# Performance work log

Hardware: AMD Instinct MI355X
Metric: run time of the kernel (lower is better)

## Reference

```python
import jax, jax.numpy as jnp
import numpy as np

N_NODES = 100000
IN_CH = 256
EMBED = 256
N_EDGES = 300000
EPS = 1e-5


def _glorot(key, shape):
    fan_in, fan_out = shape[0], shape[1]
    lim = (6.0 / (fan_in + fan_out)) ** 0.5
    return jax.random.uniform(key, shape, jnp.float32, -lim, lim)


def setup_inputs() -> dict:
    key = jax.random.key(0)
    ks = jax.random.split(key, 16)
    inp = {}
    inp['node_feat'] = jax.random.normal(ks[0], (N_NODES, IN_CH), jnp.float32)
    inp['src'] = jax.random.randint(ks[1], (N_EDGES,), 0, N_NODES, jnp.int32)
    inp['dst'] = jax.random.randint(ks[2], (N_EDGES,), 0, N_NODES, jnp.int32)
    inp['neg'] = jax.random.randint(ks[3], (N_EDGES,), 0, N_NODES, jnp.int32)
    # GCNConv weights (x @ W + b), 3 layers
    inp['W1'] = _glorot(ks[4], (IN_CH, EMBED)); inp['b1'] = jnp.zeros((EMBED,), jnp.float32)
    inp['W2'] = _glorot(ks[5], (EMBED, EMBED)); inp['b2'] = jnp.zeros((EMBED,), jnp.float32)
    inp['W3'] = _glorot(ks[6], (EMBED, EMBED)); inp['b3'] = jnp.zeros((EMBED,), jnp.float32)
    # BatchNorm affine params (2 BN layers)
    inp['g1'] = jnp.ones((EMBED,), jnp.float32); inp['be1'] = jnp.zeros((EMBED,), jnp.float32)
    inp['g2'] = jnp.ones((EMBED,), jnp.float32); inp['be2'] = jnp.zeros((EMBED,), jnp.float32)
    # LinkPredictor MLP
    inp['fc1_w'] = _glorot(ks[7], (2 * EMBED, EMBED)); inp['fc1_b'] = jnp.zeros((EMBED,), jnp.float32)
    inp['fc2_w'] = _glorot(ks[8], (EMBED, 1)); inp['fc2_b'] = jnp.zeros((1,), jnp.float32)
    return inp


def gcn_conv(x, W, b, src, dst, n):
    # PyG GCNConv: out = D^{-1/2} (A + I) D^{-1/2} (x @ W) + b
    xw = x @ W
    loops = jnp.arange(n, dtype=src.dtype)
    src_l = jnp.concatenate([src, loops])
    dst_l = jnp.concatenate([dst, loops])
    deg = jax.ops.segment_sum(jnp.ones_like(dst_l, jnp.float32), dst_l, num_segments=n)
    dinv = jnp.where(deg > 0, jax.lax.rsqrt(deg), 0.0)
    norm = dinv[src_l] * dinv[dst_l]  # [E+N]
    msg = norm[:, None] * xw[src_l]   # [E+N, d]
    out = jax.ops.segment_sum(msg, dst_l, num_segments=n)
    return out + b


def batch_norm(x, g, b):
    # training-mode BN over node dim, biased variance (torch semantics)
    mu = jnp.mean(x, axis=0)
    var = jnp.mean((x - mu) ** 2, axis=0)
    return (x - mu) * jax.lax.rsqrt(var + EPS) * g + b


def link_pred(z_a, z_b, fc1_w, fc1_b, fc2_w, fc2_b):
    h = jnp.concatenate([z_a, z_b], axis=1) @ fc1_w + fc1_b
    h = jax.nn.relu(h)
    return jax.nn.sigmoid(h @ fc2_w + fc2_b).reshape(-1)


def reference(node_feat, src, dst, neg, W1, b1, W2, b2, W3, b3, g1, be1, g2, be2, fc1_w, fc1_b, fc2_w, fc2_b):
    n = node_feat.shape[0]
    # encoder (dropout p used only in training; inference/deterministic here)
    x = gcn_conv(node_feat, W1, b1, src, dst, n)
    x = jax.nn.relu(batch_norm(x, g1, be1))
    x = gcn_conv(x, W2, b2, src, dst, n)
    x = jax.nn.relu(batch_norm(x, g2, be2))
    z = gcn_conv(x, W3, b3, src, dst, n)
    z_src, z_dst, z_neg = z[src], z[dst], z[neg]
    pos_out = link_pred(z_src, z_dst, fc1_w, fc1_b, fc2_w, fc2_b)
    neg_out = link_pred(z_src, z_neg, fc1_w, fc1_b, fc2_w, fc2_b)
    return (pos_out, neg_out)
```

## Files before the change

kernel.cpp:

```cpp
#include <hip/hip_runtime.h>
#include <hip/hip_bf16.h>

#define N_NODES 100000
#define N_EDGES 300000
#define CH 256
#define EPS 1e-5f
#define AGG_BLOCKS 3125
#define Y_TILES 782
#define Y_TILES_PAD 784

typedef __hip_bfloat16 bf16;
typedef __attribute__((ext_vector_type(8))) short bf16x8_t;
typedef __attribute__((ext_vector_type(4))) float f32x4_t;

__device__ __forceinline__ unsigned short f2bf(float f) {
    bf16 h = __float2bfloat16(f);
    return __builtin_bit_cast(unsigned short, h);
}
__device__ __forceinline__ float bf2f(unsigned short u) {
    unsigned int x = ((unsigned int)u) << 16;
    return __builtin_bit_cast(float, x);
}
__device__ __forceinline__ float bflo(unsigned int w) {
    return __builtin_bit_cast(float, w << 16);
}
__device__ __forceinline__ float bfhi(unsigned int w) {
    return __builtin_bit_cast(float, w & 0xffff0000u);
}
__device__ __forceinline__ unsigned pack2(float a, float b) {
    return (unsigned)f2bf(a) | ((unsigned)f2bf(b) << 16);
}
__device__ __forceinline__ void store_val(bf16* p, float v) { *p = __float2bfloat16(v); }

__device__ __forceinline__ void async_copy16(const void* g, void* l) {
    __builtin_amdgcn_global_load_lds((const __attribute__((address_space(1))) void*)g,
                                     (__attribute__((address_space(3))) void*)l, 16, 0, 0);
}

__global__ void k_zero_int(int* __restrict__ p, int n) {
    int i = blockIdx.x * 256 + threadIdx.x;
    if (i < n) p[i] = 0;
}
__global__ void k_count_deg(const int* __restrict__ dst, int* __restrict__ deg) {
    int e = blockIdx.x * 256 + threadIdx.x;
    if (e < N_EDGES) atomicAdd(&deg[dst[e]], 1);
}
__global__ void k_dinv_from_deg(const int* __restrict__ deg, float* __restrict__ dinv) {
    int i = blockIdx.x * 256 + threadIdx.x;
    if (i < N_NODES) dinv[i] = rsqrtf((float)(deg[i] + 1));
}
__global__ void k_block_sums(const int* __restrict__ deg, int* __restrict__ bsum) {
    __shared__ int s[256];
    int t = threadIdx.x;
    int i = blockIdx.x * 256 + t;
    s[t] = (i < N_NODES) ? deg[i] : 0;
    __syncthreads();
    for (int off = 128; off > 0; off >>= 1) {
        if (t < off) s[t] += s[t + off];
        __syncthreads();
    }
    if (t == 0) bsum[blockIdx.x] = s[0];
}
__global__ void k_scan_bsums(int* __restrict__ bsum, int nb) {
    __shared__ int s[512];
    int t = threadIdx.x;
    int v = (t < nb) ? bsum[t] : 0;
    s[t] = v;
    __syncthreads();
    for (int off = 1; off < 512; off <<= 1) {
        int u = (t >= off) ? s[t - off] : 0;
        __syncthreads();
        s[t] += u;
        __syncthreads();
    }
    if (t < nb) bsum[t] = s[t] - v;
}
__global__ void k_row_ptr(const int* __restrict__ deg, const int* __restrict__ bsum,
                          int* __restrict__ row_ptr) {
    __shared__ int s[256];
    int t = threadIdx.x;
    int i = blockIdx.x * 256 + t;
    int v = (i < N_NODES) ? deg[i] : 0;
    s[t] = v;
    __syncthreads();
    for (int off = 1; off < 256; off <<= 1) {
        int u = (t >= off) ? s[t - off] : 0;
        __syncthreads();
        s[t] += u;
        __syncthreads();
    }
    if (i < N_NODES) row_ptr[i] = bsum[blockIdx.x] + s[t] - v;
    if (blockIdx.x == 0 && t == 0) row_ptr[N_NODES] = N_EDGES;
}
__global__ void k_scatter(const int* __restrict__ src, const int* __restrict__ dst,
                          const int* __restrict__ row_ptr, int* __restrict__ cursor,
                          const float* __restrict__ dinv,
                          int* __restrict__ col, float* __restrict__ wedge,
                          int* __restrict__ eid, int* __restrict__ rowid) {
    int e = blockIdx.x * 256 + threadIdx.x;
    if (e < N_EDGES) {
        int d = dst[e], s = src[e];
        int p = atomicAdd(&cursor[d], 1);
        int idx = row_ptr[d] + p;
        col[idx] = s;
        wedge[idx] = dinv[d] * dinv[s];
        eid[idx] = e;
        rowid[idx] = d;
    }
}

__global__ void k_transpose_all(const float* __restrict__ W1, const float* __restrict__ W2,
                                bf16* __restrict__ wt) {
    int which = blockIdx.x >> 8;
    int idx = ((blockIdx.x & 255) << 8) + threadIdx.x;
    int n = idx >> 8, k = idx & 255;
    const float* W = which ? W2 : W1;
    wt[(size_t)which * 65536 + (size_t)n * 256 + k] =
        __float2bfloat16(W[(size_t)k * 256 + n]);
}

__global__ void k_fuse_w(const float* __restrict__ W3, const float* __restrict__ fc1w,
                         bf16* __restrict__ wtf) {
    __shared__ float w3row[256];
    int k = blockIdx.x;
    int n = threadIdx.x;
    if (n < 256) w3row[n] = W3[(size_t)k * 256 + n];
    __syncthreads();
    int nc = n & 255;
    size_t ro = (n < 256) ? 0 : 256;
    float acc = 0.f;
#pragma unroll 4
    for (int j = 0; j < 256; ++j)
        acc += w3row[j] * fc1w[(ro + j) * 256 + nc];
    wtf[(size_t)n * 256 + k] = __float2bfloat16(acc);
}
__global__ void k_fuse_bias(const float* __restrict__ b3, const float* __restrict__ fc1w,
                            const float* __restrict__ fc1b, float* __restrict__ bout) {
    int n = threadIdx.x;
    int nc = n & 255;
    size_t ro = (n < 256) ? 0 : 256;
    float acc = (n < 256) ? fc1b[n] : 0.f;
#pragma unroll 4
    for (int j = 0; j < 256; ++j)
        acc += b3[j] * fc1w[(ro + j) * 256 + nc];
    bout[n] = acc;
}

__global__ void k_cast_bf16_v4(const float* __restrict__ x, unsigned short* __restrict__ y) {
    int i = blockIdx.x * 256 + threadIdx.x;
    float4 v = ((const float4*)x)[i];
    ushort4 o;
    o.x = f2bf(v.x); o.y = f2bf(v.y); o.z = f2bf(v.z); o.w = f2bf(v.w);
    ((ushort4*)y)[i] = o;
}

template <int NX, bool BIAS, bool STATS>
__global__ __launch_bounds__(256) void k_gemm_mfma(const bf16* __restrict__ A,
                                                   const bf16* __restrict__ Bt,
                                                   bf16* __restrict__ C, int M, int ldc,
                                                   const float* __restrict__ bias,
                                                   float* __restrict__ part) {
    constexpr int LOG2NX = (NX == 4) ? 2 : 1;
    int id = blockIdx.x;
    int rg = (id & 7) + 8 * (id >> (3 + LOG2NX));
    int ct = (id >> 3) & (NX - 1);
    if (rg >= Y_TILES) return;
    const int row0 = rg * 128;
    const int col0 = ct * 128;

    __shared__ bf16 As[128 * 64];
    __shared__ bf16 Bs[128 * 64];
    __shared__ float sS[2][128];
    __shared__ float sQ[2][128];
    const int tid = threadIdx.x;
    const int lane = tid & 63;
    const int w = tid >> 6;
    const int wr = w >> 1, wc = w & 1;
    const int lr = lane & 15, quad = lane >> 4;

    f32x4_t acc[4][4] = {};

    for (int k0 = 0; k0 < 256; k0 += 64) {
#pragma unroll
        for (int i = 0; i < 4; ++i) {
            int j = i * 256 + tid;
            int r = j >> 3, c = j & 7;
            int gk = ((c ^ (r & 7)) << 3);
            int gr = row0 + r; gr = gr < M ? gr : M - 1;
            async_copy16(A + (size_t)gr * 256 + k0 + gk, (void*)(As + j * 8));
            async_copy16(Bt + (size_t)(col0 + r) * 256 + k0 + gk, (void*)(Bs + j * 8));
        }
        __syncthreads();
#pragma unroll
        for (int ks = 0; ks < 2; ++ks) {
            bf16x8_t af[4], bfr[4];
#pragma unroll
            for (int mi = 0; mi < 4; ++mi) {
                int m = wr * 64 + mi * 16 + lr;
                int c = (ks * 4 + quad) ^ (m & 7);
                af[mi] = *(const bf16x8_t*)(As + m * 64 + c * 8);
            }
#pragma unroll
            for (int ni = 0; ni < 4; ++ni) {
                int n = wc * 64 + ni * 16 + lr;
                int c = (ks * 4 + quad) ^ (n & 7);
                bfr[ni] = *(const bf16x8_t*)(Bs + n * 64 + c * 8);
            }
#pragma unroll
            for (int mi = 0; mi < 4; ++mi)
#pragma unroll
                for (int ni = 0; ni < 4; ++ni)
                    acc[mi][ni] = __builtin_amdgcn_mfma_f32_16x16x32_bf16(
                        af[mi], bfr[ni], acc[mi][ni], 0, 0, 0);
        }
        __syncthreads();
    }
#pragma unroll
    for (int ni = 0; ni < 4; ++ni) {
        int colg = col0 + wc * 64 + ni * 16 + lr;
        float bv = BIAS ? bias[colg] : 0.f;
#pragma unroll
        for (int mi = 0; mi < 4; ++mi)
#pragma unroll
            for (int r = 0; r < 4; ++r) acc[mi][ni][r] += bv;
    }
    if (STATS) {
        float cs[4] = {}, cq[4] = {};
#pragma unroll
        for (int mi = 0; mi < 4; ++mi)
#pragma unroll
            for (int r = 0; r < 4; ++r) {
                int row = row0 + wr * 64 + mi * 16 + quad * 4 + r;
                if (row < M) {
#pragma unroll
                    for (int ni = 0; ni < 4; ++ni) {
                        float v = acc[mi][ni][r];
                        cs[ni] += v;
                        cq[ni] += v * v;
                    }
                }
            }
#pragma unroll
        for (int ni = 0; ni < 4; ++ni) {
            cs[ni] += __shfl_xor(cs[ni], 16, 64);
            cs[ni] += __shfl_xor(cs[ni], 32, 64);
            cq[ni] += __shfl_xor(cq[ni], 16, 64);
            cq[ni] += __shfl_xor(cq[ni], 32, 64);
        }
        if (quad == 0) {
#pragma unroll
            for (int ni = 0; ni < 4; ++ni) {
                int cc = wc * 64 + ni * 16 + lr;
                sS[wr][cc] = cs[ni];
                sQ[wr][cc] = cq[ni];
            }
        }
        __syncthreads();
        if (tid < 128) {
            float ss = sS[0][tid] + sS[1][tid];
            float qq = sQ[0][tid] + sQ[1][tid];
            int cg = col0 + tid;
            part[(size_t)rg * 512 + cg] = ss;
            part[(size_t)rg * 512 + 256 + cg] = qq;
        }
    }
#pragma unroll
    for (int mi = 0; mi < 4; ++mi) {
#pragma unroll
        for (int r = 0; r < 4; ++r) {
            int row = row0 + wr * 64 + mi * 16 + quad * 4 + r;
            if (row < M) {
#pragma unroll
                for (int ni = 0; ni < 4; ++ni) {
                    int colg = col0 + wc * 64 + ni * 16 + lr;
                    store_val(C + (size_t)row * ldc + colg, acc[mi][ni][r]);
                }
            }
        }
    }
}

template <bool BN>
__device__ __forceinline__ void expand8(uint4 m, const float* sc, const float* sh, float* r) {
    r[0] = bflo(m.x); r[1] = bfhi(m.x); r[2] = bflo(m.y); r[3] = bfhi(m.y);
    r[4] = bflo(m.z); r[5] = bfhi(m.z); r[6] = bflo(m.w); r[7] = bfhi(m.w);
    if (BN) {
#pragma unroll
        for (int i = 0; i < 8; ++i) r[i] = fmaxf(r[i] * sc[i] + sh[i], 0.f);
    }
}

template <bool BN>
__global__ __launch_bounds__(256) void k_agg_csr(const unsigned short* __restrict__ x,
                                                 const int* __restrict__ row_ptr,
                                                 const int* __restrict__ col,
                                                 const float* __restrict__ wedge,
                                                 const float* __restrict__ dinv,
                                                 const float* __restrict__ scale,
                                                 const float* __restrict__ shift,
                                                 bf16* __restrict__ out) {
    int g = threadIdx.x >> 5, lh = threadIdx.x & 31;
    int base = blockIdx.x * 32 + g * 4;
    const uint4* xv = (const uint4*)x;
    float sc[8], sh[8];
    if (BN) {
        float4 a = ((const float4*)scale)[lh * 2];
        float4 b = ((const float4*)scale)[lh * 2 + 1];
        float4 c = ((const float4*)shift)[lh * 2];
        float4 d = ((const float4*)shift)[lh * 2 + 1];
        sc[0] = a.x; sc[1] = a.y; sc[2] = a.z; sc[3] = a.w;
        sc[4] = b.x; sc[5] = b.y; sc[6] = b.z; sc[7] = b.w;
        sh[0] = c.x; sh[1] = c.y; sh[2] = c.z; sh[3] = c.w;
        sh[4] = d.x; sh[5] = d.y; sh[6] = d.z; sh[7] = d.w;
    }
#pragma unroll
    for (int n = 0; n < 4; ++n) {
        int node = base + n;
        int beg = row_ptr[node], end = row_ptr[node + 1];
        float dv = dinv[node];
        float s2 = dv * dv;
        uint4 xr = xv[(size_t)node * 32 + lh];
        float rs[8];
        expand8<BN>(xr, sc, sh, rs);
        float a[8];
#pragma unroll
        for (int t = 0; t < 8; ++t) a[t] = s2 * rs[t];
        int i = beg;
        for (; i + 2 <= end; i += 2) {
            int sa = col[i], sb = col[i + 1];
            float wa = wedge[i], wb = wedge[i + 1];
            uint4 ma = xv[(size_t)sa * 32 + lh];
            uint4 mb = xv[(size_t)sb * 32 + lh];
            float ra[8], rb[8];
            expand8<BN>(ma, sc, sh, ra);
            expand8<BN>(mb, sc, sh, rb);
#pragma unroll
            for (int t = 0; t < 8; ++t) a[t] += wa * ra[t] + wb * rb[t];
        }
        if (i < end) {
            int sa = col[i];
            float wa = wedge[i];
            uint4 ma = xv[(size_t)sa * 32 + lh];
            float ra[8];
            expand8<BN>(ma, sc, sh, ra);
#pragma unroll
            for (int t = 0; t < 8; ++t) a[t] += wa * ra[t];
        }
        uint4 o;
        o.x = pack2(a[0], a[1]); o.y = pack2(a[2], a[3]);
        o.z = pack2(a[4], a[5]); o.w = pack2(a[6], a[7]);
        ((uint4*)(out + (size_t)node * CH))[lh] = o;
    }
}

__global__ __launch_bounds__(256) void k_bn_finalize(const float* __restrict__ part,
                                                     const float* __restrict__ g,
                                                     const float* __restrict__ be,
                                                     float* __restrict__ scale,
                                                     float* __restrict__ shift) {
    int wave = threadIdx.x >> 6, lane = threadIdx.x & 63;
    int c = blockIdx.x * 4 + wave;
    float s = 0.f, q = 0.f;
    for (int j = lane; j < Y_TILES; j += 64) {
        s += part[(size_t)j * 512 + c];
        q += part[(size_t)j * 512 + 256 + c];
    }
#pragma unroll
    for (int off = 32; off > 0; off >>= 1) {
        s += __shfl_down(s, off, 64);
        q += __shfl_down(q, off, 64);
    }
    if (lane == 0) {
        float mu = s * (1.0f / N_NODES);
        float var = q * (1.0f / N_NODES) - mu * mu;
        float sc = g[c] * rsqrtf(var + EPS);
        scale[c] = sc;
        shift[c] = be[c] - mu * sc;
    }
}

__global__ __launch_bounds__(256) void k_edge_score(
        const unsigned short* __restrict__ uv,
        const int* __restrict__ col, const int* __restrict__ eid,
        const int* __restrict__ rowid, const int* __restrict__ neg,
        const float* __restrict__ fc2_w, const float* __restrict__ fc2_b,
        float* __restrict__ out) {
    constexpr int NWG = 18750;
    constexpr int Q = NWG / 8, R = NWG % 8;
    int bid = blockIdx.x;
    int xcd = bid & 7, ord = bid >> 3;
    int swz = ((xcd < R) ? xcd * (Q + 1) : R * (Q + 1) + (xcd - R) * Q) + ord;
    int wave = threadIdx.x >> 6, lane = threadIdx.x & 63;
    int qtr = lane >> 4, l = lane & 15;
    int i = swz * 16 + wave * 4 + qtr;
    int s = col[i], d = rowid[i], e = eid[i];
    int g = neg[e];
    const uint4* uvv = (const uint4*)uv;
    uint4 u0 = uvv[(size_t)s * 64 + l * 2];
    uint4 u1 = uvv[(size_t)s * 64 + l * 2 + 1];
    uint4 p0 = uvv[(size_t)d * 64 + 32 + l * 2];
    uint4 p1 = uvv[(size_t)d * 64 + 33 + l * 2];
    uint4 n0 = uvv[(size_t)g * 64 + 32 + l * 2];
    uint4 n1 = uvv[(size_t)g * 64 + 33 + l * 2];
    float4 w0 = ((const float4*)fc2_w)[l * 4];
    float4 w1 = ((const float4*)fc2_w)[l * 4 + 1];
    float4 w2 = ((const float4*)fc2_w)[l * 4 + 2];
    float4 w3 = ((const float4*)fc2_w)[l * 4 + 3];

    float t0 = bflo(u0.x), t1 = bfhi(u0.x), t2 = bflo(u0.y), t3 = bfhi(u0.y);
    float t4 = bflo(u0.z), t5 = bfhi(u0.z), t6 = bflo(u0.w), t7 = bfhi(u0.w);
    float t8 = bflo(u1.x), t9 = bfhi(u1.x), ta = bflo(u1.y), tb = bfhi(u1.y);
    float tc = bflo(u1.z), td = bfhi(u1.z), te = bflo(u1.w), tf = bfhi(u1.w);

    float accp =
        fmaxf(t0 + bflo(p0.x), 0.f) * w0.x + fmaxf(t1 + bfhi(p0.x), 0.f) * w0.y +
        fmaxf(t2 + bflo(p0.y), 0.f) * w0.z + fmaxf(t3 + bfhi(p0.y), 0.f) * w0.w +
        fmaxf(t4 + bflo(p0.z), 0.f) * w1.x + fmaxf(t5 + bfhi(p0.z), 0.f) * w1.y +
        fmaxf(t6 + bflo(p0.w), 0.f) * w1.z + fmaxf(t7 + bfhi(p0.w), 0.f) * w1.w +
        fmaxf(t8 + bflo(p1.x), 0.f) * w2.x + fmaxf(t9 + bfhi(p1.x), 0.f) * w2.y +
        fmaxf(ta + bflo(p1.y), 0.f) * w2.z + fmaxf(tb + bfhi(p1.y), 0.f) * w2.w +
        fmaxf(tc + bflo(p1.z), 0.f) * w3.x + fmaxf(td + bfhi(p1.z), 0.f) * w3.y +
        fmaxf(te + bflo(p1.w), 0.f) * w3.z + fmaxf(tf + bfhi(p1.w), 0.f) * w3.w;
    float accn =
        fmaxf(t0 + bflo(n0.x), 0.f) * w0.x + fmaxf(t1 + bfhi(n0.x), 0.f) * w0.y +
        fmaxf(t2 + bflo(n0.y), 0.f) * w0.z + fmaxf(t3 + bfhi(n0.y), 0.f) * w0.w +
        fmaxf(t4 + bflo(n0.z), 0.f) * w1.x + fmaxf(t5 + bfhi(n0.z), 0.f) * w1.y +
        fmaxf(t6 + bflo(n0.w), 0.f) * w1.z + fmaxf(t7 + bfhi(n0.w), 0.f) * w1.w +
        fmaxf(t8 + bflo(n1.x), 0.f) * w2.x + fmaxf(t9 + bfhi(n1.x), 0.f) * w2.y +
        fmaxf(ta + bflo(n1.y), 0.f) * w2.z + fmaxf(tb + bfhi(n1.y), 0.f) * w2.w +
        fmaxf(tc + bflo(n1.z), 0.f) * w3.x + fmaxf(td + bfhi(n1.z), 0.f) * w3.y +
        fmaxf(te + bflo(n1.w), 0.f) * w3.z + fmaxf(tf + bfhi(n1.w), 0.f) * w3.w;
#pragma unroll
    for (int off = 8; off > 0; off >>= 1) {
        accp += __shfl_down(accp, off, 64);
        accn += __shfl_down(accn, off, 64);
    }
    if (l == 0) {
        float bb = fc2_b[0];
        out[e] = 1.0f / (1.0f + expf(-(accp + bb)));
        out[N_EDGES + e] = 1.0f / (1.0f + expf(-(accn + bb)));
    }
}

extern "C" void kernel_launch(void* const* d_in, const int* in_sizes, int n_in,
                              void* d_out, int out_size, void* d_ws, size_t ws_size,
                              hipStream_t stream) {
    const float* node_feat = (const float*)d_in[0];
    const int* src = (const int*)d_in[1];
    const int* dst = (const int*)d_in[2];
    const int* neg = (const int*)d_in[3];
    const float* W1 = (const float*)d_in[4];  const float* b1 = (const float*)d_in[5];
    const float* W2 = (const float*)d_in[6];  const float* b2 = (const float*)d_in[7];
    const float* W3 = (const float*)d_in[8];  const float* b3 = (const float*)d_in[9];
    const float* g1 = (const float*)d_in[10]; const float* be1 = (const float*)d_in[11];
    const float* g2 = (const float*)d_in[12]; const float* be2 = (const float*)d_in[13];
    const float* fc1_w = (const float*)d_in[14]; const float* fc1_b = (const float*)d_in[15];
    const float* fc2_w = (const float*)d_in[16]; const float* fc2_b = (const float*)d_in[17];
    float* out = (float*)d_out;

    const size_t NF = (size_t)N_NODES * CH;
    bf16* UV = (bf16*)d_ws;
    bf16* Xbf = UV + 2 * NF;
    bf16* XwBf = Xbf + NF;
    bf16* wt = XwBf + NF;
    float* dinv = (float*)(wt + 4 * 65536);
    float* bnpart = dinv + N_NODES;
    float* scale = bnpart + (size_t)Y_TILES * 512;
    float* shift = scale + CH;
    float* b3fc = shift + CH;
    float* wedge = b3fc + 512;
    int* ideg = (int*)(wedge + N_EDGES);
    int* cursor = ideg + N_NODES;
    int* row_ptr = cursor + N_NODES;
    int* col = row_ptr + N_NODES + 1;
    int* eid = col + N_EDGES;
    int* rowid = eid + N_EDGES;
    int* bsum = rowid + N_EDGES;
    (void)ws_size;

    int gemmBlocks = 2 * Y_TILES_PAD;
    int uvBlocks = 4 * Y_TILES_PAD;
    int nodeBlocks = (N_NODES + 255) / 256;
    int edgeBlocks = (N_EDGES + 255) / 256;
    int v4Blocks = (int)(NF / 4 / 256);
    int scoreBlocks = N_EDGES / 16;

    k_zero_int<<<(2 * N_NODES + 255) / 256, 256, 0, stream>>>(ideg, 2 * N_NODES);
    k_count_deg<<<edgeBlocks, 256, 0, stream>>>(dst, ideg);
    k_dinv_from_deg<<<nodeBlocks, 256, 0, stream>>>(ideg, dinv);
    k_block_sums<<<nodeBlocks, 256, 0, stream>>>(ideg, bsum);
    k_scan_bsums<<<1, 512, 0, stream>>>(bsum, nodeBlocks);
    k_row_ptr<<<nodeBlocks, 256, 0, stream>>>(ideg, bsum, row_ptr);
    k_scatter<<<edgeBlocks, 256, 0, stream>>>(src, dst, row_ptr, cursor, dinv, col, wedge,
                                              eid, rowid);

    k_transpose_all<<<512, 256, 0, stream>>>(W1, W2, wt);
    k_fuse_w<<<256, 512, 0, stream>>>(W3, fc1_w, wt + 2 * 65536);
    k_fuse_bias<<<1, 512, 0, stream>>>(b3, fc1_w, fc1_b, b3fc);

    k_cast_bf16_v4<<<v4Blocks, 256, 0, stream>>>(node_feat, (unsigned short*)Xbf);

    k_agg_csr<false><<<AGG_BLOCKS, 256, 0, stream>>>((unsigned short*)Xbf, row_ptr, col,
                                                     wedge, dinv, nullptr, nullptr, XwBf);
    k_gemm_mfma<2, true, true><<<gemmBlocks, 256, 0, stream>>>(XwBf, wt, Xbf, N_NODES, 256,
                                                               b1, bnpart);
    k_bn_finalize<<<64, 256, 0, stream>>>(bnpart, g1, be1, scale, shift);

    k_agg_csr<true><<<AGG_BLOCKS, 256, 0, stream>>>((unsigned short*)Xbf, row_ptr, col,
                                                    wedge, dinv, scale, shift, XwBf);
    k_gemm_mfma<2, true, true><<<gemmBlocks, 256, 0, stream>>>(XwBf, wt + 65536, Xbf,
                                                               N_NODES, 256, b2, bnpart);
    k_bn_finalize<<<64, 256, 0, stream>>>(bnpart, g2, be2, scale, shift);

    k_agg_csr<true><<<AGG_BLOCKS, 256, 0, stream>>>((unsigned short*)Xbf, row_ptr, col,
                                                    wedge, dinv, scale, shift, XwBf);
    k_gemm_mfma<4, true, false><<<uvBlocks, 256, 0, stream>>>(XwBf, wt + 2 * 65536, UV,
                                                              N_NODES, 512, b3fc, nullptr);

    k_edge_score<<<scoreBlocks, 256, 0, stream>>>((unsigned short*)UV, col, eid, rowid, neg,
                                                  fc2_w, fc2_b, out);
}
```

Baseline: 566.0 us.

## Fuse input cast into first GEMM and move layer-1 BN stats into aggregation

The first layer now runs GEMM before aggregation, and the GEMM converts the fp32 node features to bf16 while loading them. That removes the separate cast kernel and its round trip through memory. Bias and the batch-norm partial sums move into the aggregation kernel, which adds shared-memory reductions and partials per aggregation block, so finalize reads more partials. Small setup kernels (dinv, fused bias) are folded into other launches to cut launch count; the synchronous fp32 A loads in the GEMM lose the async copy path.

Result: no change. 558.8 us (-1.3%).

```diff
diff --git a/kernel.cpp b/kernel.cpp
--- a/kernel.cpp
+++ b/kernel.cpp
@@ -17,10 +17,6 @@
     bf16 h = __float2bfloat16(f);
     return __builtin_bit_cast(unsigned short, h);
 }
-__device__ __forceinline__ float bf2f(unsigned short u) {
-    unsigned int x = ((unsigned int)u) << 16;
-    return __builtin_bit_cast(float, x);
-}
 __device__ __forceinline__ float bflo(unsigned int w) {
     return __builtin_bit_cast(float, w << 16);
 }
@@ -45,15 +41,14 @@
     int e = blockIdx.x * 256 + threadIdx.x;
     if (e < N_EDGES) atomicAdd(&deg[dst[e]], 1);
 }
-__global__ void k_dinv_from_deg(const int* __restrict__ deg, float* __restrict__ dinv) {
-    int i = blockIdx.x * 256 + threadIdx.x;
-    if (i < N_NODES) dinv[i] = rsqrtf((float)(deg[i] + 1));
-}
-__global__ void k_block_sums(const int* __restrict__ deg, int* __restrict__ bsum) {
+__global__ void k_block_sums(const int* __restrict__ deg, int* __restrict__ bsum,
+                             float* __restrict__ dinv) {
     __shared__ int s[256];
     int t = threadIdx.x;
     int i = blockIdx.x * 256 + t;
-    s[t] = (i < N_NODES) ? deg[i] : 0;
+    int v = (i < N_NODES) ? deg[i] : 0;
+    s[t] = v;
+    if (i < N_NODES) dinv[i] = rsqrtf((float)(v + 1));
     __syncthreads();
     for (int off = 128; off > 0; off >>= 1) {
         if (t < off) s[t] += s[t + off];
@@ -120,42 +115,33 @@
 }
 
 __global__ void k_fuse_w(const float* __restrict__ W3, const float* __restrict__ fc1w,
-                         bf16* __restrict__ wtf) {
+                         const float* __restrict__ b3, const float* __restrict__ fc1b,
+                         bf16* __restrict__ wtf, float* __restrict__ bout) {
+    int n = threadIdx.x;
+    int nc = n & 255;
+    size_t ro = (n < 256) ? 0 : 256;
+    if (blockIdx.x == 256) {
+        float acc = (n < 256) ? fc1b[n] : 0.f;
+#pragma unroll 4
+        for (int j = 0; j < 256; ++j)
+            acc += b3[j] * fc1w[(ro + j) * 256 + nc];
+        bout[n] = acc;
+        return;
+    }
     __shared__ float w3row[256];
     int k = blockIdx.x;
-    int n = threadIdx.x;
     if (n < 256) w3row[n] = W3[(size_t)k * 256 + n];
     __syncthreads();
-    int nc = n & 255;
-    size_t ro = (n < 256) ? 0 : 256;
     float acc = 0.f;
 #pragma unroll 4
     for (int j = 0; j < 256; ++j)
         acc += w3row[j] * fc1w[(ro + j) * 256 + nc];
     wtf[(size_t)n * 256 + k] = __float2bfloat16(acc);
 }
-__global__ void k_fuse_bias(const float* __restrict__ b3, const float* __restrict__ fc1w,
-                            const float* __restrict__ fc1b, float* __restrict__ bout) {
-    int n = threadIdx.x;
-    int nc = n & 255;
-    size_t ro = (n < 256) ? 0 : 256;
-    float acc = (n < 256) ? fc1b[n] : 0.f;
-#pragma unroll 4
-    for (int j = 0; j < 256; ++j)
-        acc += b3[j] * fc1w[(ro + j) * 256 + nc];
-    bout[n] = acc;
-}
-
-__global__ void k_cast_bf16_v4(const float* __restrict__ x, unsigned short* __restrict__ y) {
-    int i = blockIdx.x * 256 + threadIdx.x;
-    float4 v = ((const float4*)x)[i];
-    ushort4 o;
-    o.x = f2bf(v.x); o.y = f2bf(v.y); o.z = f2bf(v.z); o.w = f2bf(v.w);
-    ((ushort4*)y)[i] = o;
-}
-
-template <int NX, bool BIAS, bool STATS>
+
+template <int NX, bool BIAS, bool STATS, bool F32A>
 __global__ __launch_bounds__(256) void k_gemm_mfma(const bf16* __restrict__ A,
+                                                   const float* __restrict__ Af,
                                                    const bf16* __restrict__ Bt,
                                                    bf16* __restrict__ C, int M, int ldc,
                                                    const float* __restrict__ bias,
@@ -187,7 +173,16 @@
             int r = j >> 3, c = j & 7;
             int gk = ((c ^ (r & 7)) << 3);
             int gr = row0 + r; gr = gr < M ? gr : M - 1;
-            async_copy16(A + (size_t)gr * 256 + k0 + gk, (void*)(As + j * 8));
+            if (F32A) {
+                const float4* ap = (const float4*)(Af + (size_t)gr * 256 + k0 + gk);
+                float4 fa = ap[0], fb = ap[1];
+                uint4 o;
+                o.x = pack2(fa.x, fa.y); o.y = pack2(fa.z, fa.w);
+                o.z = pack2(fb.x, fb.y); o.w = pack2(fb.z, fb.w);
+                *(uint4*)(As + (size_t)j * 8) = o;
+            } else {
+                async_copy16(A + (size_t)gr * 256 + k0 + gk, (void*)(As + j * 8));
+            }
             async_copy16(Bt + (size_t)(col0 + r) * 256 + k0 + gk, (void*)(Bs + j * 8));
         }
         __syncthreads();
@@ -290,7 +285,7 @@
     }
 }
 
-template <bool BN>
+template <bool BN, bool STATS>
 __global__ __launch_bounds__(256) void k_agg_csr(const unsigned short* __restrict__ x,
                                                  const int* __restrict__ row_ptr,
                                                  const int* __restrict__ col,
@@ -298,11 +293,15 @@
                                                  const float* __restrict__ dinv,
                                                  const float* __restrict__ scale,
                                                  const float* __restrict__ shift,
-                                                 bf16* __restrict__ out) {
+                                                 const float* __restrict__ bias,
+                                                 bf16* __restrict__ out,
+                                                 float* __restrict__ part) {
+    __shared__ float sred[8][256];
+    __shared__ float qred[8][256];
     int g = threadIdx.x >> 5, lh = threadIdx.x & 31;
     int base = blockIdx.x * 32 + g * 4;
     const uint4* xv = (const uint4*)x;
-    float sc[8], sh[8];
+    float sc[8], sh[8], bs[8];
     if (BN) {
         float4 a = ((const float4*)scale)[lh * 2];
         float4 b = ((const float4*)scale)[lh * 2 + 1];
@@ -313,6 +312,13 @@
         sh[0] = c.x; sh[1] = c.y; sh[2] = c.z; sh[3] = c.w;
         sh[4] = d.x; sh[5] = d.y; sh[6] = d.z; sh[7] = d.w;
     }
+    if (STATS) {
+        float4 e = ((const float4*)bias)[lh * 2];
+        float4 f = ((const float4*)bias)[lh * 2 + 1];
+        bs[0] = e.x; bs[1] = e.y; bs[2] = e.z; bs[3] = e.w;
+        bs[4] = f.x; bs[5] = f.y; bs[6] = f.z; bs[7] = f.w;
+    }
+    float s8[8] = {}, q8[8] = {};
 #pragma unroll
     for (int n = 0; n < 4; ++n) {
         int node = base + n;
@@ -346,22 +352,47 @@
 #pragma unroll
             for (int t = 0; t < 8; ++t) a[t] += wa * ra[t];
         }
+        if (STATS) {
+#pragma unroll
+            for (int t = 0; t < 8; ++t) {
+                a[t] += bs[t];
+                s8[t] += a[t];
+                q8[t] += a[t] * a[t];
+            }
+        }
         uint4 o;
         o.x = pack2(a[0], a[1]); o.y = pack2(a[2], a[3]);
         o.z = pack2(a[4], a[5]); o.w = pack2(a[6], a[7]);
         ((uint4*)(out + (size_t)node * CH))[lh] = o;
     }
+    if (STATS) {
+#pragma unroll
+        for (int j = 0; j < 8; ++j) {
+            sred[g][lh * 8 + j] = s8[j];
+            qred[g][lh * 8 + j] = q8[j];
+        }
+        __syncthreads();
+        int t = threadIdx.x;
+        float ss = 0.f, qq = 0.f;
+#pragma unroll
+        for (int gg = 0; gg < 8; ++gg) {
+            ss += sred[gg][t];
+            qq += qred[gg][t];
+        }
+        part[(size_t)blockIdx.x * 512 + t] = ss;
+        part[(size_t)blockIdx.x * 512 + 256 + t] = qq;
+    }
 }
 
 __global__ __launch_bounds__(256) void k_bn_finalize(const float* __restrict__ part,
                                                      const float* __restrict__ g,
                                                      const float* __restrict__ be,
                                                      float* __restrict__ scale,
-                                                     float* __restrict__ shift) {
+                                                     float* __restrict__ shift, int npart) {
     int wave = threadIdx.x >> 6, lane = threadIdx.x & 63;
     int c = blockIdx.x * 4 + wave;
     float s = 0.f, q = 0.f;
-    for (int j = lane; j < Y_TILES; j += 64) {
+    for (int j = lane; j < npart; j += 64) {
         s += part[(size_t)j * 512 + c];
         q += part[(size_t)j * 512 + 256 + c];
     }
@@ -465,7 +496,7 @@
     bf16* wt = XwBf + NF;
     float* dinv = (float*)(wt + 4 * 65536);
     float* bnpart = dinv + N_NODES;
-    float* scale = bnpart + (size_t)Y_TILES * 512;
+    float* scale = bnpart + (size_t)AGG_BLOCKS * 512;
     float* shift = scale + CH;
     float* b3fc = shift + CH;
     float* wedge = b3fc + 512;
@@ -482,40 +513,35 @@
     int uvBlocks = 4 * Y_TILES_PAD;
     int nodeBlocks = (N_NODES + 255) / 256;
     int edgeBlocks = (N_EDGES + 255) / 256;
-    int v4Blocks = (int)(NF / 4 / 256);
     int scoreBlocks = N_EDGES / 16;
 
     k_zero_int<<<(2 * N_NODES + 255) / 256, 256, 0, stream>>>(ideg, 2 * N_NODES);
     k_count_deg<<<edgeBlocks, 256, 0, stream>>>(dst, ideg);
-    k_dinv_from_deg<<<nodeBlocks, 256, 0, stream>>>(ideg, dinv);
-    k_block_sums<<<nodeBlocks, 256, 0, stream>>>(ideg, bsum);
+    k_block_sums<<<nodeBlocks, 256, 0, stream>>>(ideg, bsum, dinv);
     k_scan_bsums<<<1, 512, 0, stream>>>(bsum, nodeBlocks);
     k_row_ptr<<<nodeBlocks, 256, 0, stream>>>(ideg, bsum, row_ptr);
     k_scatter<<<edgeBlocks, 256, 0, stream>>>(src, dst, row_ptr, cursor, dinv, col, wedge,
                                               eid, rowid);
 
     k_transpose_all<<<512, 256, 0, stream>>>(W1, W2, wt);
-    k_fuse_w<<<256, 512, 0, stream>>>(W3, fc1_w, wt + 2 * 65536);
-    k_fuse_bias<<<1, 512, 0, stream>>>(b3, fc1_w, fc1_b, b3fc);
-
-    k_cast_bf16_v4<<<v4Blocks, 256, 0, stream>>>(node_feat, (unsigned short*)Xbf);
-
-    k_agg_csr<false><<<AGG_BLOCKS, 256, 0, stream>>>((unsigned short*)Xbf, row_ptr, col,
-                                                     wedge, dinv, nullptr, nullptr, XwBf);
-    k_gemm_mfma<2, true, true><<<gemmBlocks, 256, 0, stream>>>(XwBf, wt, Xbf, N_NODES, 256,
-                                                               b1, bnpart);
-    k_bn_finalize<<<64, 256, 0, stream>>>(bnpart, g1, be1, scale, shift);
-
-    k_agg_csr<true><<<AGG_BLOCKS, 256, 0, stream>>>((unsigned short*)Xbf, row_ptr, col,
-                                                    wedge, dinv, scale, shift, XwBf);
-    k_gemm_mfma<2, true, true><<<gemmBlocks, 256, 0, stream>>>(XwBf, wt + 65536, Xbf,
-                                                               N_NODES, 256, b2, bnpart);
-    k_bn_finalize<<<64, 256, 0, stream>>>(bnpart, g2, be2, scale, shift);
-
-    k_agg_csr<true><<<AGG_BLOCKS, 256, 0, stream>>>((unsigned short*)Xbf, row_ptr, col,
-                                                    wedge, dinv, scale, shift, XwBf);
-    k_gemm_mfma<4, true, false><<<uvBlocks, 256, 0, stream>>>(XwBf, wt + 2 * 65536, UV,
-                                                              N_NODES, 512, b3fc, nullptr);
+    k_fuse_w<<<257, 512, 0, stream>>>(W3, fc1_w, b3, fc1_b, wt + 2 * 65536, b3fc);
+
+    k_gemm_mfma<2, false, false, true><<<gemmBlocks, 256, 0, stream>>>(
+        nullptr, node_feat, wt, XwBf, N_NODES, 256, nullptr, nullptr);
+    k_agg_csr<false, true><<<AGG_BLOCKS, 256, 0, stream>>>(
+        (unsigned short*)XwBf, row_ptr, col, wedge, dinv, nullptr, nullptr, b1, Xbf, bnpart);
+    k_bn_finalize<<<64, 256, 0, stream>>>(bnpart, g1, be1, scale, shift, AGG_BLOCKS);
+
+    k_agg_csr<true, false><<<AGG_BLOCKS, 256, 0, stream>>>(
+        (unsigned short*)Xbf, row_ptr, col, wedge, dinv, scale, shift, nullptr, XwBf, nullptr);
+    k_gemm_mfma<2, true, true, false><<<gemmBlocks, 256, 0, stream>>>(
+        XwBf, nullptr, wt + 65536, Xbf, N_NODES, 256, b2, bnpart);
+    k_bn_finalize<<<64, 256, 0, stream>>>(bnpart, g2, be2, scale, shift, Y_TILES);
+
+    k_agg_csr<true, false><<<AGG_BLOCKS, 256, 0, stream>>>(
+        (unsigned short*)Xbf, row_ptr, col, wedge, dinv, scale, shift, nullptr, XwBf, nullptr);
+    k_gemm_mfma<4, true, false, false><<<uvBlocks, 256, 0, stream>>>(
+        XwBf, nullptr, wt + 2 * 65536, UV, N_NODES, 512, b3fc, nullptr);
 
     k_edge_score<<<scoreBlocks, 256, 0, stream>>>((unsigned short*)UV, col, eid, rowid, neg,
                                                   fc2_w, fc2_b, out);
```
